# Kernel tuning notes

Measured on AMD Instinct MI355X. Metric: run time of the kernel, lower is better.

## Reference

```python
import jax, jax.numpy as jnp
import numpy as np

B, T, D = 4, 512, 512
NB, NH, PF, K = 2, 8, 2, 4
INNER = PF * D          # 1024
DH = INNER // NH        # 128
NC = 1000
EPS = 1e-5


def _ln(x, s, b):
    mu = x.mean(-1, keepdims=True)
    var = x.var(-1, keepdims=True)
    return (x - mu) / jnp.sqrt(var + EPS) * s + b


def _causal_conv(x, k, b):
    # x: [B,T,C], depthwise kernel k: [C,K]
    kk = k.shape[-1]
    xp = jnp.pad(x, ((0, 0), (kk - 1, 0), (0, 0)))
    t = x.shape[1]
    y = sum(xp[:, j:j + t, :] * k[:, j] for j in range(kk))
    return y + b


def _mlstm_scan(q, k, v, ip, fp):
    # q,k,v: [B,T,NH,DH]; ip,fp: [B,T,NH]
    b, t, nh, dh = q.shape
    C0 = jnp.zeros((b, nh, dh, dh), q.dtype)
    n0 = jnp.zeros((b, nh, dh), q.dtype)
    m0 = jnp.zeros((b, nh), q.dtype)

    def step(carry, xs):
        C, n, m = carry
        qt, kt, vt, ipt, fpt = xs
        fl = jax.nn.log_sigmoid(fpt)
        m_new = jnp.maximum(fl + m, ipt)
        i = jnp.exp(ipt - m_new)
        f = jnp.exp(fl + m - m_new)
        C = f[..., None, None] * C + i[..., None, None] * (vt[..., :, None] * kt[..., None, :])
        n = f[..., None] * n + i[..., None] * kt
        denom = jnp.maximum(jnp.abs(jnp.einsum('bhd,bhd->bh', n, qt)), 1.0)
        h = jnp.einsum('bhij,bhj->bhi', C, qt) / denom[..., None]
        return (C, n, m_new), h

    tm = lambda a: jnp.swapaxes(a, 0, 1)  # time-major
    _, h = jax.lax.scan(step, (C0, n0, m0), (tm(q), tm(k), tm(v), tm(ip), tm(fp)))
    return jnp.swapaxes(h, 0, 1)  # [B,T,NH,DH]


def _block(x, ln_s, ln_b, w_up, b_up, conv_k, conv_b, w_q, w_k, w_v,
           w_ig, b_ig, w_fg, b_fg, hn_s, w_down, b_down):
    b, t, d = x.shape
    xn = _ln(x, ln_s, ln_b)
    up = xn @ w_up + b_up                       # [B,T,2*INNER]
    xu, z = up[..., :INNER], up[..., INNER:]
    xc = jax.nn.silu(_causal_conv(xu, conv_k, conv_b))
    q = (xc @ w_q).reshape(b, t, NH, DH)
    k = (xc @ w_k).reshape(b, t, NH, DH) * (DH ** -0.5)
    v = (xu @ w_v).reshape(b, t, NH, DH)
    ip = xc @ w_ig + b_ig                       # [B,T,NH]
    fp = xc @ w_fg + b_fg
    h = _mlstm_scan(q, k, v, ip, fp)            # [B,T,NH,DH]
    mu = h.mean(-1, keepdims=True)
    var = h.var(-1, keepdims=True)
    h = (h - mu) / jnp.sqrt(var + EPS) * hn_s   # per-head norm, hn_s: [NH,DH]
    h = h.reshape(b, t, INNER) * jax.nn.silu(z)
    return x + h @ w_down + b_down


def setup_inputs() -> dict:
    key = jax.random.key(0)
    ks = jax.random.split(key, 24)
    g = lambda i, sh, sc: jax.random.normal(ks[i], sh, jnp.float32) * sc
    inp = {
        'x': g(0, (B, T, D), 1.0),
        'cls_token': g(1, (1, 1, D), 0.02),
        'ln_s': jnp.ones((NB, D)), 'ln_b': jnp.zeros((NB, D)),
        'w_up': g(2, (NB, D, 2 * INNER), D ** -0.5), 'b_up': jnp.zeros((NB, 2 * INNER)),
        'conv_k': g(3, (NB, INNER, K), 0.3), 'conv_b': jnp.zeros((NB, INNER)),
        'w_q': g(4, (NB, INNER, INNER), INNER ** -0.5),
        'w_k': g(5, (NB, INNER, INNER), INNER ** -0.5),
        'w_v': g(6, (NB, INNER, INNER), INNER ** -0.5),
        'w_ig': g(7, (NB, INNER, NH), INNER ** -0.5), 'b_ig': jnp.zeros((NB, NH)),
        'w_fg': g(8, (NB, INNER, NH), INNER ** -0.5),
        'b_fg': jnp.full((NB, NH), 3.0),
        'hn_s': jnp.ones((NB, NH, DH)),
        'w_down': g(9, (NB, INNER, D), INNER ** -0.5), 'b_down': jnp.zeros((NB, D)),
        'fc_ln_s': jnp.ones((D,)), 'fc_ln_b': jnp.zeros((D,)),
        'fc_w': g(10, (D, NC), D ** -0.5), 'fc_b': jnp.zeros((NC,)),
    }
    return inp


def reference(x, cls_token, ln_s, ln_b, w_up, b_up, conv_k, conv_b, w_q, w_k, w_v,
              w_ig, b_ig, w_fg, b_fg, hn_s, w_down, b_down,
              fc_ln_s, fc_ln_b, fc_w, fc_b):
    b = x.shape[0]
    # append class token at the last position ('last')
    h = jnp.concatenate([x, jnp.broadcast_to(cls_token, (b, 1, x.shape[-1]))], axis=1)
    for i in range(NB):
        h = _block(h, ln_s[i], ln_b[i], w_up[i], b_up[i], conv_k[i], conv_b[i],
                   w_q[i], w_k[i], w_v[i], w_ig[i], b_ig[i], w_fg[i], b_fg[i],
                   hn_s[i], w_down[i], b_down[i])
    cls = h[:, -1, :]
    y = jax.nn.relu(_ln(cls, fc_ln_s, fc_ln_b)) @ fc_w + fc_b
    return y
```

## Files before the change

### kernel.cpp

```cpp
#include <hip/hip_runtime.h>

#define EPSV 1e-5f
constexpr int Bsz = 4, T0 = 512, Dm = 512, NHh = 8, KK = 4;
constexpr int TT = 513;
constexpr int IN = 1024, DHd = 128, NCc = 1000;
constexpr int ROWS = Bsz * TT;
constexpr int MPAD = 2176;
constexpr int NCH = 9;

constexpr size_t WT_UP = 0;
constexpr size_t WT_Q  = WT_UP + 2048 * 512;
constexpr size_t WT_K  = WT_Q + 1024 * 1024;
constexpr size_t WT_V  = WT_K + 1024 * 1024;
constexpr size_t WT_DN = WT_V + 1024 * 1024;
constexpr size_t WT_STRIDE = WT_DN + 512 * 1024;

typedef __attribute__((ext_vector_type(8))) short bf16x8;
typedef __attribute__((ext_vector_type(4))) float f32x4;
typedef __attribute__((ext_vector_type(4))) unsigned short ushort4v;
typedef __attribute__((ext_vector_type(8))) unsigned short ushort8v;
typedef unsigned short u16;

__device__ __forceinline__ float siluf(float x) { return x / (1.f + __expf(-x)); }
__device__ __forceinline__ u16 f2bf(float f) {
    unsigned int u = __float_as_uint(f);
    u = (u + 0x7FFFu + ((u >> 16) & 1u)) >> 16;
    return (u16)u;
}
__device__ __forceinline__ float bfu(u16 u) {
    return __uint_as_float(((unsigned int)u) << 16);
}
__device__ __forceinline__ void gload16(const u16* g, u16* l) {
    __builtin_amdgcn_global_load_lds(
        (const __attribute__((address_space(1))) void*)g,
        (__attribute__((address_space(3))) void*)l, 16, 0, 0);
}

__global__ __launch_bounds__(256) void concat_kernel(const float* __restrict__ x,
                                                     const float* __restrict__ cls,
                                                     float* __restrict__ h) {
    int idx = blockIdx.x * 256 + threadIdx.x;
    if (idx >= Bsz * TT * Dm) return;
    int d = idx & (Dm - 1);
    int bt = idx >> 9;
    int t = bt % TT, b = bt / TT;
    h[idx] = (t < T0) ? x[((size_t)(b * T0 + t)) * Dm + d] : cls[d];
}

__global__ __launch_bounds__(256) void ln_kernel(const float* __restrict__ in,
                                                 const float* __restrict__ s,
                                                 const float* __restrict__ bb,
                                                 u16* __restrict__ out16) {
    int row = blockIdx.x, tid = threadIdx.x;
    const float* r = in + (size_t)row * Dm;
    __shared__ float s1[4], s2[4];
    float x0 = r[tid], x1 = r[tid + 256];
    float sum = x0 + x1, sq = x0 * x0 + x1 * x1;
#pragma unroll
    for (int o = 32; o > 0; o >>= 1) { sum += __shfl_xor(sum, o); sq += __shfl_xor(sq, o); }
    if ((tid & 63) == 0) { s1[tid >> 6] = sum; s2[tid >> 6] = sq; }
    __syncthreads();
    sum = s1[0] + s1[1] + s1[2] + s1[3];
    sq  = s2[0] + s2[1] + s2[2] + s2[3];
    float mu = sum / Dm, var = sq / Dm - mu * mu, inv = rsqrtf(var + EPSV);
    out16[(size_t)row * Dm + tid]       = f2bf((x0 - mu) * inv * s[tid] + bb[tid]);
    out16[(size_t)row * Dm + tid + 256] = f2bf((x1 - mu) * inv * s[tid + 256] + bb[tid + 256]);
}

__global__ __launch_bounds__(256) void w_transpose_kernel(const float* __restrict__ wup,
        const float* __restrict__ wq, const float* __restrict__ wk,
        const float* __restrict__ wv, const float* __restrict__ wdn,
        u16* __restrict__ wt) {
    int y = blockIdx.y;
    int blk = y / 5, sel = y - blk * 5;
    int Kd, N; const float* src; size_t doff;
    if (sel == 0)      { Kd = 512;  N = 2048; src = wup + (size_t)blk * 512 * 2048; doff = WT_UP; }
    else if (sel == 1) { Kd = 1024; N = 1024; src = wq  + (size_t)blk * 1024 * 1024; doff = WT_Q; }
    else if (sel == 2) { Kd = 1024; N = 1024; src = wk  + (size_t)blk * 1024 * 1024; doff = WT_K; }
    else if (sel == 3) { Kd = 1024; N = 1024; src = wv  + (size_t)blk * 1024 * 1024; doff = WT_V; }
    else               { Kd = 1024; N = 512;  src = wdn + (size_t)blk * 1024 * 512;  doff = WT_DN; }
    u16* dst = wt + (size_t)blk * WT_STRIDE + doff;
    int ntx = N >> 5;
    int ntiles = ntx * (Kd >> 5);
    int ti = blockIdx.x;
    if (ti >= ntiles) return;
    int tk = ti / ntx, tn = ti - tk * ntx;
    __shared__ u16 s[32][33];
    int tx = threadIdx.x & 31, ty = threadIdx.x >> 5;
#pragma unroll
    for (int i = 0; i < 4; i++) {
        int k = tk * 32 + ty + i * 8;
        s[ty + i * 8][tx] = f2bf(src[(size_t)k * N + tn * 32 + tx]);
    }
    __syncthreads();
#pragma unroll
    for (int i = 0; i < 4; i++) {
        int n = tn * 32 + ty + i * 8;
        dst[(size_t)n * Kd + tk * 32 + tx] = s[tx][ty + i * 8];
    }
}

template<int BM, int BN>
__device__ __forceinline__ void gemm_tile_body(const u16* __restrict__ A, int lda,
                                               const u16* __restrict__ Wt, int Kd,
                                               const float* __restrict__ bias,
                                               const float* __restrict__ resid, int ldr,
                                               float* __restrict__ Cout, int ldc,
                                               int M, float scale, int m0, int n0,
                                               u16 (*As)[BM][40], u16 (*Bs)[BN][40]) {
    constexpr int MT = BM / 32;
    constexpr int NT = BN / 32;
    constexpr int ANV = BM / 64;
    constexpr int BNV = BN / 64;
    int tid = threadIdx.x;
    int wave = tid >> 6, lane = tid & 63;
    int wm = (wave >> 1) * (BM / 2), wn = (wave & 1) * (BN / 2);
    int lrow = lane & 15, lquad = lane >> 4;

    f32x4 acc[MT][NT];
#pragma unroll
    for (int i = 0; i < MT; i++)
#pragma unroll
        for (int j = 0; j < NT; j++)
#pragma unroll
            for (int r = 0; r < 4; r++) acc[i][j][r] = 0.f;

    int am, ak, bn, bk;
    if (BM == 128) { am = tid >> 1; ak = (tid & 1) * 16; }
    else           { am = tid >> 2; ak = (tid & 3) * 8; }
    if (BN == 128) { bn = tid & 127; bk = (tid >> 7) * 16; }
    else           { bn = tid & 63;  bk = (tid >> 6) * 8; }
    int gm = m0 + am;
    const u16* arow = A + (size_t)(gm < M ? gm : 0) * lda + ak;
    bool avalid = gm < M;
    const u16* wrow = Wt + (size_t)(n0 + bn) * Kd + bk;

    ushort8v areg[ANV];
    ushort8v breg[BNV];

    auto load_tile = [&](int k0) {
        if (avalid) {
#pragma unroll
            for (int i = 0; i < ANV; i++) areg[i] = *(const ushort8v*)(arow + k0 + i * 8);
        } else {
#pragma unroll
            for (int i = 0; i < ANV; i++) areg[i] = (ushort8v){0,0,0,0,0,0,0,0};
        }
#pragma unroll
        for (int i = 0; i < BNV; i++) breg[i] = *(const ushort8v*)(wrow + k0 + i * 8);
    };
    auto store_tile = [&](int buf) {
#pragma unroll
        for (int i = 0; i < ANV; i++)
            *(ushort8v*)&As[buf][am][ak + i * 8] = areg[i];
#pragma unroll
        for (int i = 0; i < BNV; i++)
            *(ushort8v*)&Bs[buf][bn][bk + i * 8] = breg[i];
    };

    load_tile(0);
    store_tile(0);
    __syncthreads();

    int nk = Kd >> 5;
#pragma unroll 1
    for (int it = 0; it < nk; it++) {
        int cur = it & 1;
        bool more = (it + 1 < nk);
        if (more) load_tile((it + 1) << 5);
        bf16x8 afr[MT], bfr[NT];
#pragma unroll
        for (int mt = 0; mt < MT; mt++)
            afr[mt] = *(const bf16x8*)&As[cur][wm + mt * 16 + lrow][lquad * 8];
#pragma unroll
        for (int nt = 0; nt < NT; nt++)
            bfr[nt] = *(const bf16x8*)&Bs[cur][wn + nt * 16 + lrow][lquad * 8];
#pragma unroll
        for (int mt = 0; mt < MT; mt++)
#pragma unroll
            for (int nt = 0; nt < NT; nt++)
                acc[mt][nt] = __builtin_amdgcn_mfma_f32_16x16x32_bf16(
                    afr[mt], bfr[nt], acc[mt][nt], 0, 0, 0);
        if (more) store_tile(cur ^ 1);
        __syncthreads();
    }

#pragma unroll
    for (int mt = 0; mt < MT; mt++) {
#pragma unroll
        for (int r = 0; r < 4; r++) {
            int gmr = m0 + wm + mt * 16 + lquad * 4 + r;
            if (gmr >= M) continue;
#pragma unroll
            for (int nt = 0; nt < NT; nt++) {
                int gn = n0 + wn + nt * 16 + lrow;
                float v = acc[mt][nt][r] * scale;
                if (bias) v += bias[gn];
                if (resid) v += resid[(size_t)gmr * ldr + gn];
                Cout[(size_t)gmr * ldc + gn] = v;
            }
        }
    }
}

template<int BM, int BN>
__global__ __launch_bounds__(256, 2) void gemm_mfma_kernel(const u16* __restrict__ A, int lda,
                                                           const u16* __restrict__ Wt, int Kd,
                                                           const float* __restrict__ bias,
                                                           const float* __restrict__ resid, int ldr,
                                                           float* __restrict__ Cout, int ldc,
                                                           int M, float scale) {
    __shared__ __align__(16) u16 As[2][BM][40];
    __shared__ __align__(16) u16 Bs[2][BN][40];
    gemm_tile_body<BM, BN>(A, lda, Wt, Kd, bias, resid, ldr, Cout, ldc, M, scale,
                           blockIdx.y * BM, blockIdx.x * BN, As, Bs);
}

template<bool OUT16>
__device__ __forceinline__ void gemm128_body(const u16* __restrict__ A, int lda,
                                             const u16* __restrict__ Wt, int Kd,
                                             const float* __restrict__ bias,
                                             void* __restrict__ Cout, int ldc,
                                             int M, float scale, int m0, int n0,
                                             u16* As, u16* Bs) {
    int tid = threadIdx.x;
    int wave = tid >> 6, lane = tid & 63;
    int lrow = lane & 15, lquad = lane >> 4;
    int wm = (wave >> 1) * 64, wn = (wave & 1) * 64;

    const u16* ag0 = A + (size_t)(m0 + wave * 16 + (lane >> 2)) * lda + (lane & 3) * 8;
    const u16* ag1 = ag0 + (size_t)64 * lda;
    const u16* bg0 = Wt + (size_t)(n0 + wave * 16 + (lane >> 2)) * Kd + (lane & 3) * 8;
    const u16* bg1 = bg0 + (size_t)64 * Kd;

    auto stage = [&](int buf, int k0) {
        u16* a = As + buf * 4096 + wave * 512;
        u16* bb = Bs + buf * 4096 + wave * 512;
        gload16(ag0 + k0, a);
        gload16(ag1 + k0, a + 2048);
        gload16(bg0 + k0, bb);
        gload16(bg1 + k0, bb + 2048);
    };

    f32x4 acc[4][4];
#pragma unroll
    for (int i = 0; i < 4; i++)
#pragma unroll
        for (int j = 0; j < 4; j++)
#pragma unroll
            for (int r = 0; r < 4; r++) acc[i][j][r] = 0.f;

    int nk = Kd >> 5;
    stage(0, 0);
    __syncthreads();
#pragma unroll 1
    for (int it = 0; it < nk; it++) {
        int cur = it & 1;
        if (it + 1 < nk) stage(cur ^ 1, (it + 1) << 5);
        const u16* Ac = As + cur * 4096;
        const u16* Bc = Bs + cur * 4096;
        bf16x8 afr[4], bfr[4];
#pragma unroll
        for (int mt = 0; mt < 4; mt++)
            afr[mt] = *(const bf16x8*)&Ac[(wm + mt * 16 + lrow) * 32 + lquad * 8];
#pragma unroll
        for (int nt = 0; nt < 4; nt++)
            bfr[nt] = *(const bf16x8*)&Bc[(wn + nt * 16 + lrow) * 32 + lquad * 8];
#pragma unroll
        for (int mt = 0; mt < 4; mt++)
#pragma unroll
            for (int nt = 0; nt < 4; nt++)
                acc[mt][nt] = __builtin_amdgcn_mfma_f32_16x16x32_bf16(
                    afr[mt], bfr[nt], acc[mt][nt], 0, 0, 0);
        __syncthreads();
    }

#pragma unroll
    for (int mt = 0; mt < 4; mt++) {
#pragma unroll
        for (int r = 0; r < 4; r++) {
            int gmr = m0 + wm + mt * 16 + lquad * 4 + r;
            if (gmr >= M) continue;
#pragma unroll
            for (int nt = 0; nt < 4; nt++) {
                int gn = n0 + wn + nt * 16 + lrow;
                float v = acc[mt][nt][r] * scale;
                if (bias) v += bias[gn];
                if (OUT16) ((u16*)Cout)[(size_t)gmr * ldc + gn] = f2bf(v);
                else       ((float*)Cout)[(size_t)gmr * ldc + gn] = v;
            }
        }
    }
}

__global__ __launch_bounds__(256, 2) void up_gl_kernel(const u16* __restrict__ A,
        const u16* __restrict__ Wt, const float* __restrict__ bias, float* __restrict__ C) {
    __shared__ __align__(16) u16 As[2 * 4096];
    __shared__ __align__(16) u16 Bs[2 * 4096];
    gemm128_body<false>(A, Dm, Wt, Dm, bias, C, 2 * IN, ROWS, 1.f,
                        blockIdx.y * 128, blockIdx.x * 128, As, Bs);
}

__global__ __launch_bounds__(256, 2) void qkv_gl_kernel(const u16* __restrict__ xc16,
                                                        const u16* __restrict__ xu16,
                                                        const u16* __restrict__ wtblk,
                                                        u16* __restrict__ fq,
                                                        u16* __restrict__ fk,
                                                        u16* __restrict__ fv,
                                                        float kscale) {
    __shared__ __align__(16) u16 As[2 * 4096];
    __shared__ __align__(16) u16 Bs[2 * 4096];
    int sel = blockIdx.x >> 3, nx = blockIdx.x & 7;
    const u16* A = (sel == 2) ? xu16 : xc16;
    const u16* Wt = wtblk + ((sel == 0) ? WT_Q : (sel == 1) ? WT_K : WT_V);
    u16* C = (sel == 0) ? fq : (sel == 1) ? fk : fv;
    float scale = (sel == 1) ? kscale : 1.f;
    gemm128_body<true>(A, IN, Wt, IN, nullptr, C, IN, ROWS, scale,
                       blockIdx.y * 128, nx * 128, As, Bs);
}

__global__ __launch_bounds__(256) void convgates_kernel(const float* __restrict__ up,
        const float* __restrict__ ck, const float* __restrict__ cb,
        const float* __restrict__ wt, const float* __restrict__ big,
        const float* __restrict__ bfg,
        u16* __restrict__ xc16, u16* __restrict__ xu16,
        float* __restrict__ ip, float* __restrict__ fp) {
    int row = blockIdx.x, tid = threadIdx.x;
    int b = row / TT, t = row - b * TT;
    __shared__ float sx[IN];
    int c0 = tid * 4;
    float4 cur = *(const float4*)(up + (size_t)row * (2 * IN) + c0);
    float a0 = cb[c0 + 0] + cur.x * ck[(c0 + 0) * KK + 3];
    float a1 = cb[c0 + 1] + cur.y * ck[(c0 + 1) * KK + 3];
    float a2 = cb[c0 + 2] + cur.z * ck[(c0 + 2) * KK + 3];
    float a3 = cb[c0 + 3] + cur.w * ck[(c0 + 3) * KK + 3];
#pragma unroll
    for (int j = 0; j < KK - 1; j++) {
        int tt2 = t - (KK - 1) + j;
        if (tt2 >= 0) {
            float4 pv = *(const float4*)(up + ((size_t)(b * TT + tt2)) * (2 * IN) + c0);
            a0 += pv.x * ck[(c0 + 0) * KK + j];
            a1 += pv.y * ck[(c0 + 1) * KK + j];
            a2 += pv.z * ck[(c0 + 2) * KK + j];
            a3 += pv.w * ck[(c0 + 3) * KK + j];
        }
    }
    float s0 = siluf(a0), s1v = siluf(a1), s2v = siluf(a2), s3v = siluf(a3);
    *(float4*)&sx[c0] = make_float4(s0, s1v, s2v, s3v);
    ushort4v xc4 = {f2bf(s0), f2bf(s1v), f2bf(s2v), f2bf(s3v)};
    *(ushort4v*)&xc16[(size_t)row * IN + c0] = xc4;
    ushort4v xu4 = {f2bf(cur.x), f2bf(cur.y), f2bf(cur.z), f2bf(cur.w)};
    *(ushort4v*)&xu16[(size_t)row * IN + c0] = xu4;
    __syncthreads();

    int g = tid >> 4, l = tid & 15;
    const float* wrow = wt + g * IN;
    float acc = 0.f;
#pragma unroll
    for (int j = 0; j < 16; j++) {
        int k = j * 64 + l * 4;
        float4 w4 = *(const float4*)(wrow + k);
        float4 x4 = *(const float4*)&sx[k];
        acc += w4.x * x4.x + w4.y * x4.y + w4.z * x4.z + w4.w * x4.w;
    }
#pragma unroll
    for (int o = 8; o > 0; o >>= 1) acc += __shfl_down(acc, o, 16);
    if (l == 0) {
        if (g < 8) ip[(size_t)row * NHh + g] = acc + big[g];
        else       fp[(size_t)row * NHh + (g - 8)] = acc + bfg[g - 8];
    }
}

__global__ __launch_bounds__(64) void gate_scan_kernel(const float* __restrict__ ip,
        const float* __restrict__ fp, float* __restrict__ gG, float* __restrict__ gM,
        float* __restrict__ gMb, float* __restrict__ gDec) {
    constexpr int PER = 9;
    int chain = blockIdx.x;
    int b = chain >> 3, h = chain & 7;
    int lane = threadIdx.x;
    int tbase = lane * PER;
    float lcs[PER];
    float gi[PER];
    float csum = 0.f;
#pragma unroll
    for (int i = 0; i < PER; i++) {
        int t = tbase + i;
        float fpv = 0.f, ipv = 0.f;
        if (t < TT) {
            size_t gidx = (size_t)(b * TT + t) * NHh + h;
            fpv = fp[gidx]; ipv = ip[gidx];
        }
        float flv = (fpv >= 0.f) ? -log1pf(__expf(-fpv)) : (fpv - log1pf(__expf(fpv)));
        if (t >= TT) flv = 0.f;
        csum += flv;
        lcs[i] = csum;
        gi[i] = ipv;
    }
    float ps = csum;
#pragma unroll
    for (int o = 1; o < 64; o <<= 1) {
        float v = __shfl_up(ps, o);
        if (lane >= o) ps += v;
    }
    float Fexcl = ps - csum;
    float G[PER];
    float cmax = -1e30f;
#pragma unroll
    for (int i = 0; i < PER; i++) {
        int t = tbase + i;
        G[i] = (t < TT) ? (gi[i] - (Fexcl + lcs[i])) : -1e30f;
        cmax = fmaxf(cmax, G[i]);
        lcs[i] = cmax;
    }
    float pm = cmax;
#pragma unroll
    for (int o = 1; o < 64; o <<= 1) {
        float v = __shfl_up(pm, o);
        if (lane >= o) pm = fmaxf(pm, v);
    }
    float Me = __shfl_up(pm, 1);
    if (lane == 0) Me = -1e30f;
    __shared__ float sMb[NCH];
#pragma unroll
    for (int i = 0; i < PER; i++) {
        int t = tbase + i;
        if (t < TT) {
            float Mt = fmaxf(0.f, fmaxf(Me, lcs[i]));
            gG[chain * TT + t] = G[i];
            gM[chain * TT + t] = Mt;
            if (((t & 63) == 63) || t == TT - 1) sMb[t >> 6] = Mt;
        }
    }
    __syncthreads();
    if (lane < NCH) {
        float Mb = sMb[lane];
        float Mbp = (lane == 0) ? 0.f : sMb[lane - 1];
        gMb[chain * NCH + lane] = Mb;
        gDec[chain * NCH + lane] = __expf(Mbp - Mb);
    }
}

__global__ __launch_bounds__(256, 2) void chunk_state_kernel(const u16* __restrict__ kk,
        const u16* __restrict__ vv, const float* __restrict__ gG,
        const float* __restrict__ gMb, float* __restrict__ P, float* __restrict__ nP) {
    int c = blockIdx.x, chain = blockIdx.y;
    int b = chain >> 3, h = chain & 7;
    int t0 = c * 64;
    int nvalid = min(64, TT - t0);
    __shared__ __align__(16) u16 sWv[128][72];
    __shared__ __align__(16) u16 sKt[128][72];
    __shared__ float sw[64];
    int tid = threadIdx.x;
    if (tid < 64) {
        float Mb = gMb[chain * NCH + c];
        sw[tid] = (tid < nvalid) ? __expf(gG[chain * TT + t0 + tid] - Mb) : 0.f;
    }
    __syncthreads();

    {
        int j = tid >> 2, d0 = (tid & 3) * 32;
        bool val = j < nvalid;
        float wj = sw[j];
        size_t gb = ((size_t)(b * TT + t0 + j)) * IN + h * DHd + d0;
        ushort8v z8 = {0,0,0,0,0,0,0,0};
#pragma unroll
        for (int i = 0; i < 4; i++) {
            ushort8v k8 = val ? *(const ushort8v*)(kk + gb + i * 8) : z8;
            ushort8v v8 = val ? *(const ushort8v*)(vv + gb + i * 8) : z8;
#pragma unroll
            for (int e = 0; e < 8; e++) {
                int dd = d0 + i * 8 + e;
                int jc = j ^ (((dd >> 5) & 3) << 4);
                sKt[dd][jc] = k8[e];
                sWv[dd][jc] = f2bf(bfu(v8[e]) * wj);
            }
        }
    }
    __syncthreads();

    int wave = tid >> 6, lane = tid & 63;
    int lrow = lane & 15, lquad = lane >> 4;
    int wm = (wave >> 1) * 64, wn = (wave & 1) * 64;
    f32x4 acc[4][4];
#pragma unroll
    for (int mt = 0; mt < 4; mt++)
#pragma unroll
        for (int nt = 0; nt < 4; nt++)
#pragma unroll
            for (int r = 0; r < 4; r++) acc[mt][nt][r] = 0.f;

#pragma unroll
    for (int ks = 0; ks < 2; ks++) {
        bf16x8 af[4], bfr[4];
#pragma unroll
        for (int mt = 0; mt < 4; mt++) {
            int r = wm + mt * 16 + lrow;
            int g = (ks * 4 + lquad) ^ (((r >> 5) & 3) << 1);
            af[mt] = *(const bf16x8*)&sWv[r][g * 8];
        }
#pragma unroll
        for (int nt = 0; nt < 4; nt++) {
            int r = wn + nt * 16 + lrow;
            int g = (ks * 4 + lquad) ^ (((r >> 5) & 3) << 1);
            bfr[nt] = *(const bf16x8*)&sKt[r][g * 8];
        }
#pragma unroll
        for (int mt = 0; mt < 4; mt++)
#pragma unroll
            for (int nt = 0; nt < 4; nt++)
                acc[mt][nt] = __builtin_amdgcn_mfma_f32_16x16x32_bf16(
                    af[mt], bfr[nt], acc[mt][nt], 0, 0, 0);
    }

    float* Pbase = P + (((size_t)(c * 32 + chain)) << 14);
#pragma unroll
    for (int mt = 0; mt < 4; mt++)
#pragma unroll
        for (int r = 0; r < 4; r++) {
            int e = wm + mt * 16 + lquad * 4 + r;
#pragma unroll
            for (int nt = 0; nt < 4; nt++) {
                int d = wn + nt * 16 + lrow;
                Pbase[(size_t)e * 128 + d] = acc[mt][nt][r];
            }
        }

    {
        int d = tid >> 1, jh = (tid & 1) * 32;
        int swz = ((d >> 5) & 3) << 4;
        float an = 0.f;
#pragma unroll
        for (int j = 0; j < 32; j++) {
            int jj = jh + j;
            an += sw[jj] * bfu(sKt[d][jj ^ swz]);
        }
        an += __shfl_xor(an, 1);
        if ((tid & 1) == 0) nP[(size_t)(c * 32 + chain) * 128 + d] = an;
    }
}

__global__ __launch_bounds__(256) void chunk_combine_kernel(const float* __restrict__ P,
        u16* __restrict__ CB, float* __restrict__ nP, const float* __restrict__ gDec) {
    int chain = blockIdx.x >> 6;
    int seg = blockIdx.x & 63;
    int idx = seg * 256 + threadIdx.x;
    float run = 0.f;
    for (int c = 0; c < NCH; c++) {
        size_t a = (((size_t)(c * 32 + chain)) << 14) + idx;
        float tmp = P[a];
        CB[a] = f2bf(run);
        run = run * gDec[chain * NCH + c] + tmp;
    }
    if (seg == 0 && threadIdx.x < 128) {
        int d = threadIdx.x;
        float rn = 0.f;
        for (int c = 0; c < NCH; c++) {
            size_t a = (size_t)(c * 32 + chain) * 128 + d;
            float tmp = nP[a];
            nP[a] = rn;
            rn = rn * gDec[chain * NCH + c] + tmp;
        }
    }
}

__global__ __launch_bounds__(512, 2) void chunk_out_kernel(const u16* __restrict__ qq,
        const u16* __restrict__ kk, const u16* __restrict__ vv,
        const float* __restrict__ gG, const float* __restrict__ gM,
        const float* __restrict__ gMb, const u16* __restrict__ CB,
        const float* __restrict__ nP, const float* __restrict__ hn,
        const float* __restrict__ up, u16* __restrict__ out16) {
    int c = blockIdx.x, chain = blockIdx.y;
    int b = chain >> 3, h = chain & 7;
    int t0 = c * 64;
    int nvalid = min(64, TT - t0);
    __shared__ __align__(16) u16 smem[30720];
    __shared__ float sG[64], sM[64], sWr[64], sInv[64], sNb[128], sRS[2][64];
    u16* sQ  = smem;
    u16* sCB = smem + 8704;
    u16* sK  = smem + 8704;
    u16* sVt = smem;
    u16* sD  = smem + 26112;
    float* hv = (float*)smem;
    int tid = threadIdx.x;
    int wave = tid >> 6, lane = tid & 63;
    int lrow = lane & 15, lquad = lane >> 4;
    int mq = wave >> 1, nh = wave & 1;

    float Mbprev = (c > 0) ? gMb[chain * NCH + c - 1] : 0.f;
    if (tid < 64) {
        bool val = tid < nvalid;
        sG[tid] = val ? gG[chain * TT + t0 + tid] : -1e30f;
        float Mv = val ? gM[chain * TT + t0 + tid] : 1e30f;
        sM[tid] = Mv;
        sWr[tid] = val ? __expf(Mbprev - Mv) : 0.f;
    }
    if (tid >= 128 && tid < 256) sNb[tid - 128] = nP[(size_t)(c * 32 + chain) * 128 + (tid - 128)];

    ushort8v z8 = {0,0,0,0,0,0,0,0};
    {
        int lr = tid >> 3, c0 = (tid & 7) * 16;
        bool val = lr < nvalid;
        size_t gb = ((size_t)(b * TT + t0 + lr)) * IN + h * DHd + c0;
#pragma unroll
        for (int i = 0; i < 2; i++)
            *(ushort8v*)&sQ[lr * 136 + c0 + i * 8] =
                val ? *(const ushort8v*)(qq + gb + i * 8) : z8;
    }
    {
        const u16* CBbase = CB + (((size_t)(c * 32 + chain)) << 14);
        int e = tid >> 2, d0 = (tid & 3) * 32;
#pragma unroll
        for (int i = 0; i < 4; i++)
            *(ushort8v*)&sCB[e * 136 + d0 + i * 8] =
                *(const ushort8v*)(CBbase + (size_t)e * 128 + d0 + i * 8);
    }
    __syncthreads();

    f32x4 acc[4];
#pragma unroll
    for (int tt = 0; tt < 4; tt++)
#pragma unroll
        for (int r = 0; r < 4; r++) acc[tt][r] = 0.f;
#pragma unroll 1
    for (int ks = 0; ks < 4; ks++) {
        bf16x8 af = *(const bf16x8*)&sQ[(mq * 16 + lrow) * 136 + ks * 32 + lquad * 8];
#pragma unroll
        for (int tt = 0; tt < 4; tt++) {
            bf16x8 bf = *(const bf16x8*)&sCB[(nh * 64 + tt * 16 + lrow) * 136 + ks * 32 + lquad * 8];
            acc[tt] = __builtin_amdgcn_mfma_f32_16x16x32_bf16(af, bf, acc[tt], 0, 0, 0);
        }
    }
#pragma unroll
    for (int tt = 0; tt < 4; tt++)
#pragma unroll
        for (int r = 0; r < 4; r++) acc[tt][r] *= sWr[mq * 16 + lquad * 4 + r];
    __syncthreads();

    {
        int lr = tid >> 3, c0 = (tid & 7) * 16;
        bool val = lr < nvalid;
        size_t gb = ((size_t)(b * TT + t0 + lr)) * IN + h * DHd + c0;
#pragma unroll
        for (int i = 0; i < 2; i++)
            *(ushort8v*)&sK[lr * 136 + c0 + i * 8] =
                val ? *(const ushort8v*)(kk + gb + i * 8) : z8;
    }
    __syncthreads();

    {
        f32x4 accS[2];
#pragma unroll
        for (int tt = 0; tt < 2; tt++)
#pragma unroll
            for (int r = 0; r < 4; r++) accS[tt][r] = 0.f;
#pragma unroll 1
        for (int ks = 0; ks < 4; ks++) {
            bf16x8 af = *(const bf16x8*)&sQ[(mq * 16 + lrow) * 136 + ks * 32 + lquad * 8];
#pragma unroll
            for (int tt = 0; tt < 2; tt++) {
                bf16x8 bf = *(const bf16x8*)&sK[((nh * 2 + tt) * 16 + lrow) * 136 + ks * 32 + lquad * 8];
                accS[tt] = __builtin_amdgcn_mfma_f32_16x16x32_bf16(af, bf, accS[tt], 0, 0, 0);
            }
        }
        float rsum[4] = {0.f, 0.f, 0.f, 0.f};
#pragma unroll
        for (int tt = 0; tt < 2; tt++) {
            int j = (nh * 2 + tt) * 16 + lrow;
            float Gj = sG[j];
#pragma unroll
            for (int r = 0; r < 4; r++) {
                int t = mq * 16 + lquad * 4 + r;
                float w = (j <= t) ? __expf(Gj - sM[t]) : 0.f;
                float wD = accS[tt][r] * w;
                rsum[r] += wD;
                sD[t * 72 + j] = f2bf(wD);
            }
        }
#pragma unroll
        for (int r = 0; r < 4; r++) {
#pragma unroll
            for (int msk = 1; msk < 16; msk <<= 1) rsum[r] += __shfl_xor(rsum[r], msk);
        }
        if (lrow == 0) {
#pragma unroll
            for (int r = 0; r < 4; r++) sRS[nh][mq * 16 + lquad * 4 + r] = rsum[r];
        }
    }
    __syncthreads();

    if (tid < 64) {
        float qn = 0.f;
#pragma unroll 1
        for (int d4 = 0; d4 < 32; d4++) {
            ushort4v q4 = *(const ushort4v*)&sQ[tid * 136 + d4 * 4];
            float4 nb = *(const float4*)&sNb[d4 * 4];
            qn += bfu(q4.x) * nb.x + bfu(q4.y) * nb.y + bfu(q4.z) * nb.z + bfu(q4.w) * nb.w;
        }
        float den = sRS[0][tid] + sRS[1][tid] + sWr[tid] * qn;
        sInv[tid] = 1.f / fmaxf(fabsf(den), 1.f);
    }
    __syncthreads();

    {
        int e = tid & 127, tg = (tid >> 7) * 16;
#pragma unroll 1
        for (int i = 0; i < 16; i++) {
            int t = tg + i;
            sVt[e * 72 + t] = (t < nvalid) ? vv[((size_t)(b * TT + t0 + t)) * IN + h * DHd + e]
                                           : (u16)0;
        }
    }
    __syncthreads();

#pragma unroll 1
    for (int ks = 0; ks < 2; ks++) {
        bf16x8 af = *(const bf16x8*)&sD[(mq * 16 + lrow) * 72 + ks * 32 + lquad * 8];
#pragma unroll
        for (int tt = 0; tt < 4; tt++) {
            bf16x8 bf = *(const bf16x8*)&sVt[(nh * 64 + tt * 16 + lrow) * 72 + ks * 32 + lquad * 8];
            acc[tt] = __builtin_amdgcn_mfma_f32_16x16x32_bf16(af, bf, acc[tt], 0, 0, 0);
        }
    }

    __syncthreads();
#pragma unroll
    for (int tt = 0; tt < 4; tt++) {
#pragma unroll
        for (int r = 0; r < 4; r++) {
            int t = mq * 16 + lquad * 4 + r;
            int e = nh * 64 + tt * 16 + lrow;
            hv[t * 132 + e] = acc[tt][r] * sInv[t];
        }
    }
    __syncthreads();
    {
        int t = tid >> 3, s = tid & 7;
        float vals[16];
        float sum = 0.f, sq = 0.f;
#pragma unroll
        for (int i = 0; i < 16; i++) {
            float v = hv[t * 132 + s * 16 + i];
            vals[i] = v; sum += v; sq += v * v;
        }
#pragma unroll
        for (int m = 1; m < 8; m <<= 1) { sum += __shfl_xor(sum, m); sq += __shfl_xor(sq, m); }
        float mu = sum / DHd, var = sq / DHd - mu * mu, inv2 = rsqrtf(var + EPSV);
        if (t < nvalid) {
            size_t bt = (size_t)(b * TT + t0 + t);
            const float* zp = up + bt * (2 * IN) + IN + h * DHd + s * 16;
            u16* op = out16 + bt * IN + h * DHd + s * 16;
#pragma unroll
            for (int i = 0; i < 16; i++) {
                float hnv = hn[h * DHd + s * 16 + i];
                op[i] = f2bf((vals[i] - mu) * inv2 * hnv * siluf(zp[i]));
            }
        }
    }
}

__global__ __launch_bounds__(256) void fc_kernel(const float* __restrict__ hbuf,
                                                 const float* __restrict__ fcls,
                                                 const float* __restrict__ fclb,
                                                 const float* __restrict__ fw,
                                                 const float* __restrict__ fb,
                                                 float* __restrict__ out) {
    __shared__ float svc[Bsz][Dm];
    __shared__ float sred[4][256];
    int tid = threadIdx.x;
    int j0 = blockIdx.x * 64;
    {
        int r = tid >> 6, lane = tid & 63;
        const float* hrow = hbuf + ((size_t)r * TT + TT - 1) * Dm;
        float v[8];
        float sum = 0.f, sq = 0.f;
#pragma unroll
        for (int k = 0; k < 8; k++) {
            v[k] = hrow[lane + k * 64];
            sum += v[k]; sq += v[k] * v[k];
        }
#pragma unroll
        for (int o = 32; o > 0; o >>= 1) { sum += __shfl_xor(sum, o); sq += __shfl_xor(sq, o); }
        float mu = sum / Dm, var = sq / Dm - mu * mu, inv = rsqrtf(var + EPSV);
#pragma unroll
        for (int k = 0; k < 8; k++) {
            int e = lane + k * 64;
            svc[r][e] = fmaxf((v[k] - mu) * inv * fcls[e] + fclb[e], 0.f);
        }
    }
    __syncthreads();
    int j = j0 + (tid & 63);
    int chunk = tid >> 6;
    int kbase = chunk * 128;
    float a0 = 0.f, a1 = 0.f, a2 = 0.f, a3 = 0.f;
    if (j < NCc) {
        const float* fwp = fw + (size_t)kbase * NCc + j;
#pragma unroll 4
        for (int kk = 0; kk < 128; kk++) {
            float w = fwp[(size_t)kk * NCc];
            a0 += svc[0][kbase + kk] * w;
            a1 += svc[1][kbase + kk] * w;
            a2 += svc[2][kbase + kk] * w;
            a3 += svc[3][kbase + kk] * w;
        }
    }
    int jl = tid & 63;
    sred[chunk][jl * 4 + 0] = a0;
    sred[chunk][jl * 4 + 1] = a1;
    sred[chunk][jl * 4 + 2] = a2;
    sred[chunk][jl * 4 + 3] = a3;
    __syncthreads();
    if (tid < 64) {
        int jj = j0 + tid;
        if (jj < NCc) {
            float bias = fb[jj];
#pragma unroll
            for (int b = 0; b < Bsz; b++) {
                float v = sred[0][tid * 4 + b] + sred[1][tid * 4 + b]
                        + sred[2][tid * 4 + b] + sred[3][tid * 4 + b];
                out[b * NCc + jj] = v + bias;
            }
        }
    }
}

__global__ __launch_bounds__(256) void gate_w_transpose(const float* __restrict__ wig,
                                                        const float* __restrict__ wfg,
                                                        float* __restrict__ wt) {
    int idx = blockIdx.x * 256 + threadIdx.x;
    int k = idx & 1023;
    int g = (idx >> 10) & 15;
    int blk = idx >> 14;
    const float* w = (g < 8) ? (wig + (size_t)blk * IN * NHh) : (wfg + (size_t)blk * IN * NHh);
    wt[idx] = w[k * NHh + (g & 7)];
}

extern "C" void kernel_launch(void* const* d_in, const int* in_sizes, int n_in,
                              void* d_out, int out_size, void* d_ws, size_t ws_size,
                              hipStream_t stream) {
    const float* x      = (const float*)d_in[0];
    const float* cls    = (const float*)d_in[1];
    const float* ln_s   = (const float*)d_in[2];
    const float* ln_b   = (const float*)d_in[3];
    const float* w_up   = (const float*)d_in[4];
    const float* b_up   = (const float*)d_in[5];
    const float* conv_k = (const float*)d_in[6];
    const float* conv_b = (const float*)d_in[7];
    const float* w_q    = (const float*)d_in[8];
    const float* w_k    = (const float*)d_in[9];
    const float* w_v    = (const float*)d_in[10];
    const float* w_ig   = (const float*)d_in[11];
    const float* b_ig   = (const float*)d_in[12];
    const float* w_fg   = (const float*)d_in[13];
    const float* b_fg   = (const float*)d_in[14];
    const float* hn_s   = (const float*)d_in[15];
    const float* w_down = (const float*)d_in[16];
    const float* b_down = (const float*)d_in[17];
    const float* fcls   = (const float*)d_in[18];
    const float* fclb   = (const float*)d_in[19];
    const float* fc_w   = (const float*)d_in[20];
    const float* fc_b   = (const float*)d_in[21];
    float* out = (float*)d_out;

    float* ws = (float*)d_ws;
    size_t off = 0;
    float* f_h  = ws + off; off += (size_t)ROWS * Dm;
    float* f_up = ws + off; off += (size_t)ROWS * 2 * IN;
    float* f_ip = ws + off; off += (size_t)ROWS * NHh;
    float* f_fp = ws + off; off += (size_t)ROWS * NHh;
    float* g_G  = ws + off; off += 32 * TT;
    float* g_M  = ws + off; off += 32 * TT;
    float* g_Mb = ws + off; off += 32 * NCH;
    float* g_De = ws + off; off += 32 * NCH;
    float* g_P  = ws + off; off += (size_t)NCH * 32 * DHd * DHd;
    float* g_nP = ws + off; off += (size_t)NCH * 32 * DHd;
    float* g_wt = ws + off; off += 2 * 16 * IN;
    u16* g_CB  = (u16*)(ws + off); off += ((size_t)NCH * 32 * DHd * DHd + 1) / 2;
    u16* g_Wt  = (u16*)(ws + off); off += (2 * WT_STRIDE + 1) / 2;
    u16* f_xn16 = (u16*)(ws + off); off += ((size_t)MPAD * Dm) / 2;
    u16* f_xc16 = (u16*)(ws + off); off += ((size_t)MPAD * IN) / 2;
    u16* f_xu16 = (u16*)(ws + off); off += ((size_t)MPAD * IN) / 2;
    u16* f_xg16 = (u16*)(ws + off); off += ((size_t)ROWS * IN + 1) / 2;
    u16* f_q16  = (u16*)(ws + off); off += ((size_t)ROWS * IN + 1) / 2;
    u16* f_k16  = (u16*)(ws + off); off += ((size_t)ROWS * IN + 1) / 2;
    u16* f_v16  = (u16*)(ws + off); off += ((size_t)ROWS * IN + 1) / 2;

    const float kscale = 0.08838834764831845f;
    const int MB = (ROWS + 127) / 128;
    const int MB64 = (ROWS + 63) / 64;

    concat_kernel<<<(ROWS * Dm + 255) / 256, 256, 0, stream>>>(x, cls, f_h);
    gate_w_transpose<<<(2 * 16 * IN + 255) / 256, 256, 0, stream>>>(w_ig, w_fg, g_wt);
    w_transpose_kernel<<<dim3(1024, 10), 256, 0, stream>>>(w_up, w_q, w_k, w_v, w_down, g_Wt);

    for (int blk = 0; blk < 2; blk++) {
        const float* p_ln_s = ln_s + blk * Dm;
        const float* p_ln_b = ln_b + blk * Dm;
        const float* p_bup  = b_up + (size_t)blk * 2 * IN;
        const float* p_ck   = conv_k + (size_t)blk * IN * KK;
        const float* p_cb   = conv_b + (size_t)blk * IN;
        const float* p_big  = b_ig + (size_t)blk * NHh;
        const float* p_bfg  = b_fg + (size_t)blk * NHh;
        const float* p_hns  = hn_s + (size_t)blk * NHh * DHd;
        const float* p_bd   = b_down + (size_t)blk * Dm;
        const u16*   p_wt   = g_Wt + (size_t)blk * WT_STRIDE;

        ln_kernel<<<ROWS, 256, 0, stream>>>(f_h, p_ln_s, p_ln_b, f_xn16);

        up_gl_kernel<<<dim3(2 * IN / 128, MB), 256, 0, stream>>>(
            f_xn16, p_wt + WT_UP, p_bup, f_up);

        convgates_kernel<<<ROWS, 256, 0, stream>>>(
            f_up, p_ck, p_cb, g_wt + blk * 16 * IN, p_big, p_bfg,
            f_xc16, f_xu16, f_ip, f_fp);

        qkv_gl_kernel<<<dim3(24, MB), 256, 0, stream>>>(
            f_xc16, f_xu16, p_wt, f_q16, f_k16, f_v16, kscale);

        gate_scan_kernel<<<32, 64, 0, stream>>>(f_ip, f_fp, g_G, g_M, g_Mb, g_De);
        chunk_state_kernel<<<dim3(NCH, 32), 256, 0, stream>>>(f_k16, f_v16, g_G, g_Mb, g_P, g_nP);
        chunk_combine_kernel<<<32 * 64, 256, 0, stream>>>(g_P, g_CB, g_nP, g_De);
        chunk_out_kernel<<<dim3(NCH, 32), 512, 0, stream>>>(f_q16, f_k16, f_v16, g_G, g_M, g_Mb,
                                                            g_CB, g_nP, p_hns, f_up, f_xg16);

        gemm_mfma_kernel<64, 64><<<dim3(Dm / 64, MB64), 256, 0, stream>>>(
            f_xg16, IN, p_wt + WT_DN, IN, p_bd, f_h, Dm, f_h, Dm, ROWS, 1.f);
    }

    fc_kernel<<<(NCc + 63) / 64, 256, 0, stream>>>(f_h, fcls, fclb, fc_w, fc_b, out);
}
```

Measured before the change: 419.1 us.

## Fuse gate scan into chunk state, concat into LN, bf16 chunk partials

```diff
diff --git a/kernel.cpp b/kernel.cpp
--- a/kernel.cpp
+++ b/kernel.cpp
@@ -36,25 +36,27 @@
         (__attribute__((address_space(3))) void*)l, 16, 0, 0);
 }
 
-__global__ __launch_bounds__(256) void concat_kernel(const float* __restrict__ x,
-                                                     const float* __restrict__ cls,
-                                                     float* __restrict__ h) {
-    int idx = blockIdx.x * 256 + threadIdx.x;
-    if (idx >= Bsz * TT * Dm) return;
-    int d = idx & (Dm - 1);
-    int bt = idx >> 9;
-    int t = bt % TT, b = bt / TT;
-    h[idx] = (t < T0) ? x[((size_t)(b * T0 + t)) * Dm + d] : cls[d];
-}
-
+template<bool CAT>
 __global__ __launch_bounds__(256) void ln_kernel(const float* __restrict__ in,
+                                                 const float* __restrict__ x,
+                                                 const float* __restrict__ cls,
                                                  const float* __restrict__ s,
                                                  const float* __restrict__ bb,
+                                                 float* __restrict__ hout,
                                                  u16* __restrict__ out16) {
     int row = blockIdx.x, tid = threadIdx.x;
-    const float* r = in + (size_t)row * Dm;
+    float x0, x1;
+    if (CAT) {
+        int b = row / TT, t = row - b * TT;
+        const float* src = (t < T0) ? (x + ((size_t)(b * T0 + t)) * Dm) : cls;
+        x0 = src[tid]; x1 = src[tid + 256];
+        hout[(size_t)row * Dm + tid] = x0;
+        hout[(size_t)row * Dm + tid + 256] = x1;
+    } else {
+        const float* r = in + (size_t)row * Dm;
+        x0 = r[tid]; x1 = r[tid + 256];
+    }
     __shared__ float s1[4], s2[4];
-    float x0 = r[tid], x1 = r[tid + 256];
     float sum = x0 + x1, sq = x0 * x0 + x1 * x1;
 #pragma unroll
     for (int o = 32; o > 0; o >>= 1) { sum += __shfl_xor(sum, o); sq += __shfl_xor(sq, o); }
@@ -70,8 +72,21 @@
 __global__ __launch_bounds__(256) void w_transpose_kernel(const float* __restrict__ wup,
         const float* __restrict__ wq, const float* __restrict__ wk,
         const float* __restrict__ wv, const float* __restrict__ wdn,
-        u16* __restrict__ wt) {
+        const float* __restrict__ wig, const float* __restrict__ wfg,
+        u16* __restrict__ wt, float* __restrict__ gwt) {
     int y = blockIdx.y;
+    if (y >= 10) {
+        int blk = y - 10;
+        int idx = blockIdx.x * 256 + threadIdx.x;
+        if (idx < 16 * IN) {
+            int k = idx & 1023;
+            int g = (idx >> 10) & 15;
+            const float* w = (g < 8) ? (wig + (size_t)blk * IN * NHh)
+                                     : (wfg + (size_t)blk * IN * NHh);
+            gwt[(size_t)blk * 16 * IN + idx] = w[k * NHh + (g & 7)];
+        }
+        return;
+    }
     int blk = y / 5, sel = y - blk * 5;
     int Kd, N; const float* src; size_t doff;
     if (sel == 0)      { Kd = 512;  N = 2048; src = wup + (size_t)blk * 512 * 2048; doff = WT_UP; }
@@ -371,78 +386,11 @@
     }
 }
 
-__global__ __launch_bounds__(64) void gate_scan_kernel(const float* __restrict__ ip,
+__global__ __launch_bounds__(256, 2) void chunk_state_kernel(const u16* __restrict__ kk,
+        const u16* __restrict__ vv, const float* __restrict__ ip,
         const float* __restrict__ fp, float* __restrict__ gG, float* __restrict__ gM,
-        float* __restrict__ gMb, float* __restrict__ gDec) {
-    constexpr int PER = 9;
-    int chain = blockIdx.x;
-    int b = chain >> 3, h = chain & 7;
-    int lane = threadIdx.x;
-    int tbase = lane * PER;
-    float lcs[PER];
-    float gi[PER];
-    float csum = 0.f;
-#pragma unroll
-    for (int i = 0; i < PER; i++) {
-        int t = tbase + i;
-        float fpv = 0.f, ipv = 0.f;
-        if (t < TT) {
-            size_t gidx = (size_t)(b * TT + t) * NHh + h;
-            fpv = fp[gidx]; ipv = ip[gidx];
-        }
-        float flv = (fpv >= 0.f) ? -log1pf(__expf(-fpv)) : (fpv - log1pf(__expf(fpv)));
-        if (t >= TT) flv = 0.f;
-        csum += flv;
-        lcs[i] = csum;
-        gi[i] = ipv;
-    }
-    float ps = csum;
-#pragma unroll
-    for (int o = 1; o < 64; o <<= 1) {
-        float v = __shfl_up(ps, o);
-        if (lane >= o) ps += v;
-    }
-    float Fexcl = ps - csum;
-    float G[PER];
-    float cmax = -1e30f;
-#pragma unroll
-    for (int i = 0; i < PER; i++) {
-        int t = tbase + i;
-        G[i] = (t < TT) ? (gi[i] - (Fexcl + lcs[i])) : -1e30f;
-        cmax = fmaxf(cmax, G[i]);
-        lcs[i] = cmax;
-    }
-    float pm = cmax;
-#pragma unroll
-    for (int o = 1; o < 64; o <<= 1) {
-        float v = __shfl_up(pm, o);
-        if (lane >= o) pm = fmaxf(pm, v);
-    }
-    float Me = __shfl_up(pm, 1);
-    if (lane == 0) Me = -1e30f;
-    __shared__ float sMb[NCH];
-#pragma unroll
-    for (int i = 0; i < PER; i++) {
-        int t = tbase + i;
-        if (t < TT) {
-            float Mt = fmaxf(0.f, fmaxf(Me, lcs[i]));
-            gG[chain * TT + t] = G[i];
-            gM[chain * TT + t] = Mt;
-            if (((t & 63) == 63) || t == TT - 1) sMb[t >> 6] = Mt;
-        }
-    }
-    __syncthreads();
-    if (lane < NCH) {
-        float Mb = sMb[lane];
-        float Mbp = (lane == 0) ? 0.f : sMb[lane - 1];
-        gMb[chain * NCH + lane] = Mb;
-        gDec[chain * NCH + lane] = __expf(Mbp - Mb);
-    }
-}
-
-__global__ __launch_bounds__(256, 2) void chunk_state_kernel(const u16* __restrict__ kk,
-        const u16* __restrict__ vv, const float* __restrict__ gG,
-        const float* __restrict__ gMb, float* __restrict__ P, float* __restrict__ nP) {
+        float* __restrict__ gMb, float* __restrict__ gDec,
+        u16* __restrict__ P16, float* __restrict__ nP) {
     int c = blockIdx.x, chain = blockIdx.y;
     int b = chain >> 3, h = chain & 7;
     int t0 = c * 64;
@@ -450,10 +398,75 @@
     __shared__ __align__(16) u16 sWv[128][72];
     __shared__ __align__(16) u16 sKt[128][72];
     __shared__ float sw[64];
+    __shared__ float sGf[TT];
+    __shared__ float sMbl[NCH];
     int tid = threadIdx.x;
+
     if (tid < 64) {
-        float Mb = gMb[chain * NCH + c];
-        sw[tid] = (tid < nvalid) ? __expf(gG[chain * TT + t0 + tid] - Mb) : 0.f;
+        constexpr int PER = 9;
+        int lane = tid;
+        int tbase = lane * PER;
+        float lcs[PER], gi[PER];
+        float csum = 0.f;
+#pragma unroll
+        for (int i = 0; i < PER; i++) {
+            int t = tbase + i;
+            float fpv = 0.f, ipv = 0.f;
+            if (t < TT) {
+                size_t gidx = (size_t)(b * TT + t) * NHh + h;
+                fpv = fp[gidx]; ipv = ip[gidx];
+            }
+            float flv = (fpv >= 0.f) ? -log1pf(__expf(-fpv)) : (fpv - log1pf(__expf(fpv)));
+            if (t >= TT) flv = 0.f;
+            csum += flv;
+            lcs[i] = csum;
+            gi[i] = ipv;
+        }
+        float ps = csum;
+#pragma unroll
+        for (int o = 1; o < 64; o <<= 1) {
+            float v = __shfl_up(ps, o);
+            if (lane >= o) ps += v;
+        }
+        float Fexcl = ps - csum;
+        float G[PER];
+        float cmax = -1e30f;
+#pragma unroll
+        for (int i = 0; i < PER; i++) {
+            int t = tbase + i;
+            G[i] = (t < TT) ? (gi[i] - (Fexcl + lcs[i])) : -1e30f;
+            cmax = fmaxf(cmax, G[i]);
+            lcs[i] = cmax;
+        }
+        float pm = cmax;
+#pragma unroll
+        for (int o = 1; o < 64; o <<= 1) {
+            float v = __shfl_up(pm, o);
+            if (lane >= o) pm = fmaxf(pm, v);
+        }
+        float Me = __shfl_up(pm, 1);
+        if (lane == 0) Me = -1e30f;
+#pragma unroll
+        for (int i = 0; i < PER; i++) {
+            int t = tbase + i;
+            if (t < TT) {
+                float Mt = fmaxf(0.f, fmaxf(Me, lcs[i]));
+                sGf[t] = G[i];
+                if (c == 0) { gG[chain * TT + t] = G[i]; gM[chain * TT + t] = Mt; }
+                if (((t & 63) == 63) || t == TT - 1) sMbl[t >> 6] = Mt;
+            }
+        }
+    }
+    __syncthreads();
+    if (c == 0 && tid < NCH) {
+        float Mbv = sMbl[tid];
+        float Mbp = (tid == 0) ? 0.f : sMbl[tid - 1];
+        gMb[chain * NCH + tid] = Mbv;
+        gDec[chain * NCH + tid] = __expf(Mbp - Mbv);
+    }
+    if (tid < 64) {
+        float Mb = sMbl[c];
+        sw[tid] = (tid < nvalid) ? __expf(sGf[t0 + tid] - Mb) : 0.f;
     }
     __syncthreads();
 
@@ -512,7 +525,7 @@
                     af[mt], bfr[nt], acc[mt][nt], 0, 0, 0);
     }
 
-    float* Pbase = P + (((size_t)(c * 32 + chain)) << 14);
+    u16* Pbase = P16 + (((size_t)(c * 32 + chain)) << 14);
 #pragma unroll
     for (int mt = 0; mt < 4; mt++)
 #pragma unroll
@@ -521,7 +534,7 @@
 #pragma unroll
             for (int nt = 0; nt < 4; nt++) {
                 int d = wn + nt * 16 + lrow;
-                Pbase[(size_t)e * 128 + d] = acc[mt][nt][r];
+                Pbase[(size_t)e * 128 + d] = f2bf(acc[mt][nt][r]);
             }
         }
 
@@ -539,7 +552,7 @@
     }
 }
 
-__global__ __launch_bounds__(256) void chunk_combine_kernel(const float* __restrict__ P,
+__global__ __launch_bounds__(256) void chunk_combine_kernel(const u16* __restrict__ P16,
         u16* __restrict__ CB, float* __restrict__ nP, const float* __restrict__ gDec) {
     int chain = blockIdx.x >> 6;
     int seg = blockIdx.x & 63;
@@ -547,7 +560,7 @@
     float run = 0.f;
     for (int c = 0; c < NCH; c++) {
         size_t a = (((size_t)(c * 32 + chain)) << 14) + idx;
-        float tmp = P[a];
+        float tmp = bfu(P16[a]);
         CB[a] = f2bf(run);
         run = run * gDec[chain * NCH + c] + tmp;
     }
@@ -821,17 +834,6 @@
             }
         }
     }
-}
-
-__global__ __launch_bounds__(256) void gate_w_transpose(const float* __restrict__ wig,
-                                                        const float* __restrict__ wfg,
-                                                        float* __restrict__ wt) {
-    int idx = blockIdx.x * 256 + threadIdx.x;
-    int k = idx & 1023;
-    int g = (idx >> 10) & 15;
-    int blk = idx >> 14;
-    const float* w = (g < 8) ? (wig + (size_t)blk * IN * NHh) : (wfg + (size_t)blk * IN * NHh);
-    wt[idx] = w[k * NHh + (g & 7)];
 }
 
 extern "C" void kernel_launch(void* const* d_in, const int* in_sizes, int n_in,
@@ -871,9 +873,9 @@
     float* g_M  = ws + off; off += 32 * TT;
     float* g_Mb = ws + off; off += 32 * NCH;
     float* g_De = ws + off; off += 32 * NCH;
-    float* g_P  = ws + off; off += (size_t)NCH * 32 * DHd * DHd;
     float* g_nP = ws + off; off += (size_t)NCH * 32 * DHd;
     float* g_wt = ws + off; off += 2 * 16 * IN;
+    u16* g_P16 = (u16*)(ws + off); off += ((size_t)NCH * 32 * DHd * DHd + 1) / 2;
     u16* g_CB  = (u16*)(ws + off); off += ((size_t)NCH * 32 * DHd * DHd + 1) / 2;
     u16* g_Wt  = (u16*)(ws + off); off += (2 * WT_STRIDE + 1) / 2;
     u16* f_xn16 = (u16*)(ws + off); off += ((size_t)MPAD * Dm) / 2;
@@ -888,9 +890,8 @@
     const int MB = (ROWS + 127) / 128;
     const int MB64 = (ROWS + 63) / 64;
 
-    concat_kernel<<<(ROWS * Dm + 255) / 256, 256, 0, stream>>>(x, cls, f_h);
-    gate_w_transpose<<<(2 * 16 * IN + 255) / 256, 256, 0, stream>>>(w_ig, w_fg, g_wt);
-    w_transpose_kernel<<<dim3(1024, 10), 256, 0, stream>>>(w_up, w_q, w_k, w_v, w_down, g_Wt);
+    w_transpose_kernel<<<dim3(1024, 12), 256, 0, stream>>>(
+        w_up, w_q, w_k, w_v, w_down, w_ig, w_fg, g_Wt, g_wt);
 
     for (int blk = 0; blk < 2; blk++) {
         const float* p_ln_s = ln_s + blk * Dm;
@@ -904,7 +905,12 @@
         const float* p_bd   = b_down + (size_t)blk * Dm;
         const u16*   p_wt   = g_Wt + (size_t)blk * WT_STRIDE;
 
-        ln_kernel<<<ROWS, 256, 0, stream>>>(f_h, p_ln_s, p_ln_b, f_xn16);
+        if (blk == 0)
+            ln_kernel<true><<<ROWS, 256, 0, stream>>>(nullptr, x, cls, p_ln_s, p_ln_b,
+                                                      f_h, f_xn16);
+        else
+            ln_kernel<false><<<ROWS, 256, 0, stream>>>(f_h, nullptr, nullptr, p_ln_s, p_ln_b,
+                                                       nullptr, f_xn16);
 
         up_gl_kernel<<<dim3(2 * IN / 128, MB), 256, 0, stream>>>(
             f_xn16, p_wt + WT_UP, p_bup, f_up);
@@ -916,9 +922,9 @@
         qkv_gl_kernel<<<dim3(24, MB), 256, 0, stream>>>(
             f_xc16, f_xu16, p_wt, f_q16, f_k16, f_v16, kscale);
 
-        gate_scan_kernel<<<32, 64, 0, stream>>>(f_ip, f_fp, g_G, g_M, g_Mb, g_De);
-        chunk_state_kernel<<<dim3(NCH, 32), 256, 0, stream>>>(f_k16, f_v16, g_G, g_Mb, g_P, g_nP);
-        chunk_combine_kernel<<<32 * 64, 256, 0, stream>>>(g_P, g_CB, g_nP, g_De);
+        chunk_state_kernel<<<dim3(NCH, 32), 256, 0, stream>>>(
+            f_k16, f_v16, f_ip, f_fp, g_G, g_M, g_Mb, g_De, g_P16, g_nP);
+        chunk_combine_kernel<<<32 * 64, 256, 0, stream>>>(g_P16, g_CB, g_nP, g_De);
         chunk_out_kernel<<<dim3(NCH, 32), 512, 0, stream>>>(f_q16, f_k16, f_v16, g_G, g_M, g_Mb,
                                                             g_CB, g_nP, p_hns, f_up, f_xg16);
 
```

Result: faster. 405.3 us (-3.3%).
